# Optimization experiments

Measured on AMD Instinct MI355X. Metric: run time of the kernel, lower is better.

## Reference

```python
import jax, jax.numpy as jnp
import numpy as np
import math

D_MODEL = 1024
N_HEADS = 16
BATCH = 2
SEQ = 2048

def setup_inputs() -> dict:
    key = jax.random.key(0)
    ks = jax.random.split(key, 5)
    d = D_MODEL
    lim_qkv = 1.0 / math.sqrt(d)
    x = jax.random.normal(ks[0], (BATCH, SEQ, d), dtype=jnp.float32)
    qkv_w = jax.random.uniform(ks[1], (3 * d, d), dtype=jnp.float32, minval=-lim_qkv, maxval=lim_qkv)
    qkv_b = jax.random.uniform(ks[2], (3 * d,), dtype=jnp.float32, minval=-lim_qkv, maxval=lim_qkv)
    out_w = jax.random.uniform(ks[3], (d, d), dtype=jnp.float32, minval=-lim_qkv, maxval=lim_qkv)
    out_b = jax.random.uniform(ks[4], (d,), dtype=jnp.float32, minval=-lim_qkv, maxval=lim_qkv)
    return {"x": x, "qkv_w": qkv_w, "qkv_b": qkv_b, "out_w": out_w, "out_b": out_b}

def reference(x, qkv_w, qkv_b, out_w, out_b):
    b, s, d = x.shape
    h = N_HEADS
    hd = d // h
    # note: original uses float division for scale: sqrt(in_features / n_heads)
    scale = math.sqrt(d / h)
    qkv = x @ qkv_w.T + qkv_b                      # [b, s, 3d]
    q, k, v = jnp.split(qkv, 3, axis=-1)           # each [b, s, d]
    def heads(t):
        return t.reshape(b, s, h, hd).transpose(0, 2, 1, 3)  # [b, h, s, hd]
    qh, kh, vh = heads(q), heads(k), heads(v)
    # faithful quirk: scores = k @ q^T (k as query, q as key)
    scores = jnp.einsum('bhid,bhjd->bhij', kh, qh) / scale   # [b, h, s, s]
    alpha = jax.nn.softmax(scores, axis=-1)
    attn = jnp.einsum('bhij,bhjd->bhid', alpha, vh)          # [b, h, s, hd]
    attn = attn.transpose(0, 2, 1, 3).reshape(b, s, d)       # [b, s, d]
    return attn @ out_w.T + out_b
```

## Files before the change

kernel.cpp:

```cpp
#include <hip/hip_runtime.h>
#include <hip/hip_fp16.h>

#define D_MODEL 1024
#define N_HEADS 16
#define HEAD_DIM 64
#define BATCH 2
#define SEQ 2048
#define ROWS (BATCH*SEQ)

#define K_SCALE 0.18033688011112042f

using h8v = __attribute__((ext_vector_type(8))) _Float16;
using h4v = __attribute__((ext_vector_type(4))) _Float16;
using g2v = __attribute__((ext_vector_type(2))) __fp16;
using g4v = __attribute__((ext_vector_type(4))) __fp16;
using us8 = __attribute__((ext_vector_type(8))) unsigned short;
using f4v = __attribute__((ext_vector_type(4))) float;

__device__ __forceinline__ ushort f2h_u(float x) { return __half_as_ushort(__float2half(x)); }
__device__ __forceinline__ void splith(float x, ushort& h, ushort& l) {
    __half hh_ = __float2half(x);
    h = __half_as_ushort(hh_);
    l = f2h_u(x - __half2float(hh_));
}

__device__ __forceinline__ size_t fidx(int row, int k) {
    return ((size_t)((row >> 7) * 32 + (k >> 5)) << 12)
         + (size_t)(((row & 127) >> 4) << 9)
         + (size_t)(((row & 15) * 4 + ((k & 31) >> 3)) << 3) + (k & 7);
}

__device__ __forceinline__ void async_lds16(const ushort* g, ushort* l) {
    __builtin_amdgcn_global_load_lds(
        (const __attribute__((address_space(1))) unsigned int*)g,
        (__attribute__((address_space(3))) unsigned int*)l, 16, 0, 0);
}

__global__ __launch_bounds__(256)
void prep_kernel(const float* __restrict__ x, const float* __restrict__ qw,
                 const float* __restrict__ ow,
                 ushort* __restrict__ xh, ushort* __restrict__ qwh,
                 ushort* __restrict__ owh, ushort* __restrict__ owl)
{
    const int b = blockIdx.x, t = threadIdx.x;
    if (b < 4096) {
        const int i = b * 256 + t;
        const int row = i >> 8, k4 = (i & 255) * 4;
        const float4 v = ((const float4*)x)[i];
        ushort4 h;
        h.x = f2h_u(v.x); h.y = f2h_u(v.y); h.z = f2h_u(v.z); h.w = f2h_u(v.w);
        *(ushort4*)&xh[fidx(row, k4)] = h;
    } else if (b < 7168) {
        const int i = (b - 4096) * 256 + t;
        const int row = i >> 8, k4 = (i & 255) * 4;
        const float4 v = ((const float4*)qw)[i];
        ushort4 h;
        h.x = f2h_u(v.x); h.y = f2h_u(v.y); h.z = f2h_u(v.z); h.w = f2h_u(v.w);
        *(ushort4*)&qwh[fidx(row, k4)] = h;
    } else {
        const int i = (b - 7168) * 256 + t;
        const int row = i >> 8, k4 = (i & 255) * 4;
        const float4 v = ((const float4*)ow)[i];
        const size_t o = fidx(row, k4);
        ushort4 h, l;
        splith(v.x, h.x, l.x); splith(v.y, h.y, l.y);
        splith(v.z, h.z, l.z); splith(v.w, h.w, l.w);
        *(ushort4*)&owh[o] = h; *(ushort4*)&owl[o] = l;
    }
}

__global__ __launch_bounds__(256, 5)
void gemm_qkv(const ushort* __restrict__ Af, const ushort* __restrict__ Wf,
              const float* __restrict__ bias,
              ushort* __restrict__ Qh, ushort* __restrict__ Kh,
              ushort* __restrict__ Vt)
{
    __shared__ ushort sA[2][4096], sW[2][2048];
    const int t = threadIdx.x, lane = t & 63, wv = t >> 6;
    const int tx = lane & 15, g = lane >> 4;
    const int lin = blockIdx.x;
    const int xcd = lin & 7, r = lin >> 3;
    const int mb = xcd * 4 + (r & 3);
    const int nb = r >> 2;
    const int at0 = (wv >> 1) * 4, wt0 = (wv & 1) * 2;
    const int fo = (tx * 4 + g) * 8;
    const size_t wbase = ((size_t)(nb & 1)) << 11;

    f4v acc[8];
#pragma unroll
    for (int i = 0; i < 8; i++)
#pragma unroll
        for (int e = 0; e < 4; e++) acc[i][e] = 0.f;

    {
        const size_t ao = ((size_t)(mb * 32)) << 12;
        const size_t wo = (((size_t)((nb >> 1) * 32)) << 12) + wbase;
#pragma unroll
        for (int c = 0; c < 2; c++) {
            const int o = (t + c * 256) * 8;
            async_lds16(Af + ao + o, &sA[0][o]);
        }
        async_lds16(Wf + wo + t * 8, &sW[0][t * 8]);
    }

    for (int kt = 0; kt < 32; kt++) {
        const int p = kt & 1;
        __syncthreads();
        if (kt < 31) {
            const size_t ao = ((size_t)(mb * 32 + kt + 1)) << 12;
            const size_t wo = (((size_t)((nb >> 1) * 32 + kt + 1)) << 12) + wbase;
#pragma unroll
            for (int c = 0; c < 2; c++) {
                const int o = (t + c * 256) * 8;
                async_lds16(Af + ao + o, &sA[p ^ 1][o]);
            }
            async_lds16(Wf + wo + t * 8, &sW[p ^ 1][t * 8]);
        }
        h8v ah[4], wh[2];
#pragma unroll
        for (int i = 0; i < 4; i++)
            ah[i] = *(const h8v*)&sA[p][(at0 + i) * 512 + fo];
#pragma unroll
        for (int i = 0; i < 2; i++)
            wh[i] = *(const h8v*)&sW[p][(wt0 + i) * 512 + fo];
        if (nb < 32) {
#pragma unroll
            for (int wi = 0; wi < 2; wi++)
#pragma unroll
                for (int ai = 0; ai < 4; ai++)
                    acc[wi * 4 + ai] = __builtin_amdgcn_mfma_f32_16x16x32_f16(wh[wi], ah[ai], acc[wi * 4 + ai], 0, 0, 0);
        } else {
#pragma unroll
            for (int ai = 0; ai < 4; ai++)
#pragma unroll
                for (int wi = 0; wi < 2; wi++)
                    acc[ai * 2 + wi] = __builtin_amdgcn_mfma_f32_16x16x32_f16(ah[ai], wh[wi], acc[ai * 2 + wi], 0, 0, 0);
        }
    }

    if (nb < 32) {
        const int part = nb >> 4;
        ushort* dst = part ? Kh : Qh;
        const float scale = part ? K_SCALE : 1.0f;
#pragma unroll
        for (int wi = 0; wi < 2; wi++) {
            const int gf0 = nb * 64 + (wv & 1) * 32 + wi * 16 + g * 4;
            const float4 bv = *(const float4*)&bias[gf0];
            const int gfl = gf0 & 1023;
            const int hh = gfl >> 6;
            const int dd = gfl & 63;
#pragma unroll
            for (int ai = 0; ai < 4; ai++) {
                const int s = mb * 128 + (wv >> 1) * 64 + ai * 16 + tx;
                const int bb = s >> 11, srel = s & 2047;
                const size_t idx = (size_t)(bb * N_HEADS + hh) * 131072
                    + (size_t)(srel >> 4) * 1024 + (size_t)(dd >> 5) * 512
                    + ((srel & 15) * 4 + ((dd & 31) >> 3)) * 8 + (dd & 7);
                const f4v a = acc[wi * 4 + ai];
                ushort4 h4;
                h4.x = f2h_u((a[0] + bv.x) * scale);
                h4.y = f2h_u((a[1] + bv.y) * scale);
                h4.z = f2h_u((a[2] + bv.z) * scale);
                h4.w = f2h_u((a[3] + bv.w) * scale);
                *(ushort4*)&dst[idx] = h4;
            }
        }
    } else {
#pragma unroll
        for (int wi = 0; wi < 2; wi++) {
            const int gf = nb * 64 + (wv & 1) * 32 + wi * 16 + tx;
            const float bv = bias[gf];
            const int gfl = gf & 1023;
            const int hh = gfl >> 6;
            const int dl = gfl & 63;
            const int t0 = mb * 2 + (wv >> 1);
            const int bb = t0 >> 5;
            const size_t base = (size_t)(bb * N_HEADS + hh) * 131072
                + (size_t)(t0 & 31) * 4096
                + (size_t)((dl >> 4) & 3) * 512
                + (size_t)g * 128 + (size_t)(dl & 15) * 8;
#pragma unroll
            for (int aip = 0; aip < 2; aip++) {
                const f4v a0 = acc[(2 * aip) * 2 + wi];
                const f4v a1 = acc[(2 * aip + 1) * 2 + wi];
                us8 s;
                s[0] = f2h_u(a0[0] + bv); s[1] = f2h_u(a0[1] + bv);
                s[2] = f2h_u(a0[2] + bv); s[3] = f2h_u(a0[3] + bv);
                s[4] = f2h_u(a1[0] + bv); s[5] = f2h_u(a1[1] + bv);
                s[6] = f2h_u(a1[2] + bv); s[7] = f2h_u(a1[3] + bv);
                *(us8*)&Vt[base + (size_t)aip * 2048] = s;
            }
        }
    }
}

__global__ __launch_bounds__(256)
void attn_mfma(const ushort* __restrict__ Kf, const ushort* __restrict__ Qf,
               const ushort* __restrict__ Vf,
               ushort* __restrict__ Oh, ushort* __restrict__ Ol)
{
    __shared__ ushort lds[32768];
    ushort* KR = lds;
    ushort* bufs = lds + 8192;

    const int t = threadIdx.x, lane = t & 63, wv = t >> 6;
    const int tx = lane & 15, g = lane >> 4;
    const int lin = blockIdx.x;
    const int xcd = lin & 7, ix = lin >> 3;
    const int bh = xcd * 4 + (ix >> 4);
    const int it = ix & 15;
    const int b = bh >> 4, h = bh & 15;
    const int i0 = it * 128;
    const size_t hb = (size_t)bh * 131072;

    {
        const size_t kb = hb + (size_t)it * 8192;
#pragma unroll
        for (int c = 0; c < 4; c++) {
            const int o = (t + c * 256) * 8;
            async_lds16(Kf + kb + o, KR + o);
        }
#pragma unroll
        for (int c = 0; c < 2; c++) {
            const int o = (t + c * 256) * 8;
            async_lds16(Qf + hb + o, bufs + o);
            async_lds16(Vf + hb + o, bufs + 4096 + o);
        }
    }
    __syncthreads();

    const int fo = (tx * 4 + g) * 8;
    const int vo = (g * 16 + tx) * 8;
    h8v kf[2][2];
#pragma unroll
    for (int is = 0; is < 2; is++)
#pragma unroll
        for (int kk = 0; kk < 2; kk++)
            kf[is][kk] = *(const h8v*)&KR[((wv * 2 + is) * 2 + kk) * 512 + fo];

    {
        const size_t off = hb + 4096;
#pragma unroll
        for (int c = 0; c < 2; c++) {
            const int o = (t + c * 256) * 8;
            async_lds16(Qf + off + o, bufs + 8192 + o);
            async_lds16(Vf + off + o, bufs + 8192 + 4096 + o);
        }
    }

    f4v O[2][4];
    float l_acc[2] = {0.f, 0.f};
#pragma unroll
    for (int is = 0; is < 2; is++)
#pragma unroll
        for (int ht = 0; ht < 4; ht++)
#pragma unroll
            for (int e = 0; e < 4; e++) O[is][ht][e] = 0.f;

    h4v php[2][4];

    {
        const ushort* sQ = bufs;
        f4v sc[2][4];
#pragma unroll
        for (int is = 0; is < 2; is++)
#pragma unroll
            for (int jn = 0; jn < 4; jn++)
#pragma unroll
                for (int e = 0; e < 4; e++) sc[is][jn][e] = 0.f;
#pragma unroll
        for (int kk = 0; kk < 2; kk++)
#pragma unroll
            for (int jn = 0; jn < 4; jn++) {
                const h8v qf = *(const h8v*)&sQ[(jn * 2 + kk) * 512 + fo];
#pragma unroll
                for (int is = 0; is < 2; is++)
                    sc[is][jn] = __builtin_amdgcn_mfma_f32_16x16x32_f16(qf, kf[is][kk], sc[is][jn], 0, 0, 0);
            }
#pragma unroll
        for (int is = 0; is < 2; is++)
#pragma unroll
            for (int jn = 0; jn < 4; jn++) {
                const float p0 = __builtin_amdgcn_exp2f(sc[is][jn][0]);
                const float p1 = __builtin_amdgcn_exp2f(sc[is][jn][1]);
                const float p2 = __builtin_amdgcn_exp2f(sc[is][jn][2]);
                const float p3 = __builtin_amdgcn_exp2f(sc[is][jn][3]);
                l_acc[is] += (p0 + p1) + (p2 + p3);
                const g2v plo = __builtin_amdgcn_cvt_pkrtz(p0, p1);
                const g2v phi = __builtin_amdgcn_cvt_pkrtz(p2, p3);
                const g4v pk = __builtin_shufflevector(plo, phi, 0, 1, 2, 3);
                php[is][jn] = __builtin_bit_cast(h4v, pk);
            }
    }

    int bp = 0, bc = 1, bn = 2;
    for (int jt = 1; jt < SEQ / 64; jt++) {
        __syncthreads();
        if (jt < SEQ / 64 - 1) {
            const size_t off = hb + (size_t)(jt + 1) * 4096;
#pragma unroll
            for (int c = 0; c < 2; c++) {
                const int o = (t + c * 256) * 8;
                async_lds16(Qf + off + o, bufs + bn * 8192 + o);
                async_lds16(Vf + off + o, bufs + bn * 8192 + 4096 + o);
            }
        }
        const ushort* sQ = bufs + bc * 8192;
        const ushort* sVp = bufs + bp * 8192 + 4096;

        f4v sc[2][4];
#pragma unroll
        for (int is = 0; is < 2; is++)
#pragma unroll
            for (int jn = 0; jn < 4; jn++)
#pragma unroll
                for (int e = 0; e < 4; e++) sc[is][jn][e] = 0.f;
#pragma unroll
        for (int kk = 0; kk < 2; kk++)
#pragma unroll
            for (int jn = 0; jn < 4; jn++) {
                const h8v qf = *(const h8v*)&sQ[(jn * 2 + kk) * 512 + fo];
#pragma unroll
                for (int is = 0; is < 2; is++)
                    sc[is][jn] = __builtin_amdgcn_mfma_f32_16x16x32_f16(qf, kf[is][kk], sc[is][jn], 0, 0, 0);
            }

#pragma unroll
        for (int jc = 0; jc < 2; jc++) {
            h8v p8[2];
#pragma unroll
            for (int is = 0; is < 2; is++)
                p8[is] = __builtin_shufflevector(php[is][jc * 2], php[is][jc * 2 + 1],
                                                 0, 1, 2, 3, 4, 5, 6, 7);
#pragma unroll
            for (int ht = 0; ht < 4; ht++) {
                const h8v vf = *(const h8v*)&sVp[jc * 2048 + ht * 512 + vo];
#pragma unroll
                for (int is = 0; is < 2; is++)
                    O[is][ht] = __builtin_amdgcn_mfma_f32_16x16x32_f16(vf, p8[is], O[is][ht], 0, 0, 0);
            }
        }

#pragma unroll
        for (int is = 0; is < 2; is++)
#pragma unroll
            for (int jn = 0; jn < 4; jn++) {
                const float p0 = __builtin_amdgcn_exp2f(sc[is][jn][0]);
                const float p1 = __builtin_amdgcn_exp2f(sc[is][jn][1]);
                const float p2 = __builtin_amdgcn_exp2f(sc[is][jn][2]);
                const float p3 = __builtin_amdgcn_exp2f(sc[is][jn][3]);
                l_acc[is] += (p0 + p1) + (p2 + p3);
                const g2v plo = __builtin_amdgcn_cvt_pkrtz(p0, p1);
                const g2v phi = __builtin_amdgcn_cvt_pkrtz(p2, p3);
                const g4v pk = __builtin_shufflevector(plo, phi, 0, 1, 2, 3);
                php[is][jn] = __builtin_bit_cast(h4v, pk);
            }

        const int tmp = bp; bp = bc; bc = bn; bn = tmp;
    }

    {
        const ushort* sVp = bufs + bp * 8192 + 4096;
#pragma unroll
        for (int jc = 0; jc < 2; jc++) {
            h8v p8[2];
#pragma unroll
            for (int is = 0; is < 2; is++)
                p8[is] = __builtin_shufflevector(php[is][jc * 2], php[is][jc * 2 + 1],
                                                 0, 1, 2, 3, 4, 5, 6, 7);
#pragma unroll
            for (int ht = 0; ht < 4; ht++) {
                const h8v vf = *(const h8v*)&sVp[jc * 2048 + ht * 512 + vo];
#pragma unroll
                for (int is = 0; is < 2; is++)
                    O[is][ht] = __builtin_amdgcn_mfma_f32_16x16x32_f16(vf, p8[is], O[is][ht], 0, 0, 0);
            }
        }
    }

#pragma unroll
    for (int is = 0; is < 2; is++) {
        float l = l_acc[is];
        l += __shfl_xor(l, 16);
        l += __shfl_xor(l, 32);
        const float inv = 1.0f / l;
        const int row = b * SEQ + i0 + (wv * 2 + is) * 16 + tx;
#pragma unroll
        for (int ht = 0; ht < 4; ht++) {
            const int k0 = h * 64 + ht * 16 + g * 4;
            const size_t o = fidx(row, k0);
            ushort4 hv, lv;
            float v;
            v = O[is][ht][0] * inv; splith(v, hv.x, lv.x);
            v = O[is][ht][1] * inv; splith(v, hv.y, lv.y);
            v = O[is][ht][2] * inv; splith(v, hv.z, lv.z);
            v = O[is][ht][3] * inv; splith(v, hv.w, lv.w);
            *(ushort4*)&Oh[o] = hv;
            *(ushort4*)&Ol[o] = lv;
        }
    }
}

__global__ __launch_bounds__(256, 4)
void gemm_out(const ushort* __restrict__ Af, const ushort* __restrict__ Alf,
              const ushort* __restrict__ Wf, const ushort* __restrict__ Wlf,
              const float* __restrict__ bias, float* __restrict__ out)
{
    __shared__ ushort sA[2][4096], sW[2][4096];
    const int t = threadIdx.x, lane = t & 63, wv = t >> 6;
    const int tx = lane & 15, g = lane >> 4;
    const int lin = blockIdx.x;
    const int xcd = lin & 7, r = lin >> 3;
    const int nb = xcd * 2 + (r & 1);
    const int mb = r >> 1;
    const int at0 = (wv >> 1) * 2, wt0 = (wv & 1) * 2;
    const int fo = (tx * 4 + g) * 8;
    const size_t abase = ((size_t)(mb & 1)) << 11;
    const size_t wbase = ((size_t)(nb & 1)) << 11;

    f4v acc[4];
#pragma unroll
    for (int i = 0; i < 4; i++)
#pragma unroll
        for (int e = 0; e < 4; e++) acc[i][e] = 0.f;

    {
        const size_t ao = (((size_t)((mb >> 1) * 32)) << 12) + abase;
        const size_t wo = (((size_t)((nb >> 1) * 32)) << 12) + wbase;
        const int o = t * 8;
        async_lds16(Af + ao + o, &sA[0][o]);
        async_lds16(Alf + ao + o, &sA[0][2048 + o]);
        async_lds16(Wf + wo + o, &sW[0][o]);
        async_lds16(Wlf + wo + o, &sW[0][2048 + o]);
    }

    for (int kt = 0; kt < 32; kt++) {
        const int p = kt & 1;
        __syncthreads();
        if (kt < 31) {
            const size_t ao = (((size_t)((mb >> 1) * 32 + kt + 1)) << 12) + abase;
            const size_t wo = (((size_t)((nb >> 1) * 32 + kt + 1)) << 12) + wbase;
            const int o = t * 8;
            async_lds16(Af + ao + o, &sA[p ^ 1][o]);
            async_lds16(Alf + ao + o, &sA[p ^ 1][2048 + o]);
            async_lds16(Wf + wo + o, &sW[p ^ 1][o]);
            async_lds16(Wlf + wo + o, &sW[p ^ 1][2048 + o]);
        }
        h8v ah[2], al[2], wh[2], wl[2];
#pragma unroll
        for (int i = 0; i < 2; i++) {
            ah[i] = *(const h8v*)&sA[p][(at0 + i) * 512 + fo];
            al[i] = *(const h8v*)&sA[p][2048 + (at0 + i) * 512 + fo];
            wh[i] = *(const h8v*)&sW[p][(wt0 + i) * 512 + fo];
            wl[i] = *(const h8v*)&sW[p][2048 + (wt0 + i) * 512 + fo];
        }
#pragma unroll
        for (int wi = 0; wi < 2; wi++)
#pragma unroll
            for (int ai = 0; ai < 2; ai++) {
                acc[wi * 2 + ai] = __builtin_amdgcn_mfma_f32_16x16x32_f16(wh[wi], ah[ai], acc[wi * 2 + ai], 0, 0, 0);
                acc[wi * 2 + ai] = __builtin_amdgcn_mfma_f32_16x16x32_f16(wh[wi], al[ai], acc[wi * 2 + ai], 0, 0, 0);
                acc[wi * 2 + ai] = __builtin_amdgcn_mfma_f32_16x16x32_f16(wl[wi], ah[ai], acc[wi * 2 + ai], 0, 0, 0);
            }
    }

#pragma unroll
    for (int wi = 0; wi < 2; wi++) {
        const int gf0 = nb * 64 + (wv & 1) * 32 + wi * 16 + g * 4;
        const float4 bv = *(const float4*)&bias[gf0];
#pragma unroll
        for (int ai = 0; ai < 2; ai++) {
            const int tok = mb * 64 + (wv >> 1) * 32 + ai * 16 + tx;
            const f4v a = acc[wi * 2 + ai];
            float4 o;
            o.x = a[0] + bv.x;
            o.y = a[1] + bv.y;
            o.z = a[2] + bv.z;
            o.w = a[3] + bv.w;
            *(float4*)&out[(size_t)tok * D_MODEL + gf0] = o;
        }
    }
}

extern "C" void kernel_launch(void* const* d_in, const int* in_sizes, int n_in,
                              void* d_out, int out_size, void* d_ws, size_t ws_size,
                              hipStream_t stream) {
    const float* x     = (const float*)d_in[0];
    const float* qkv_w = (const float*)d_in[1];
    const float* qkv_b = (const float*)d_in[2];
    const float* out_w = (const float*)d_in[3];
    const float* out_b = (const float*)d_in[4];
    float* out = (float*)d_out;

    const size_t FB = (size_t)ROWS * D_MODEL;
    const size_t MM = (size_t)D_MODEL * D_MODEL;
    ushort* u   = (ushort*)d_ws;
    ushort* xh  = u;
    ushort* Ol  = u + FB;
    ushort* Qh  = u + 2 * FB;
    ushort* Kh  = u + 3 * FB;
    ushort* Vt  = u + 4 * FB;
    ushort* qwh = u + 5 * FB;
    ushort* owh = u + 5 * FB + 3 * MM;
    ushort* owl = owh + MM;

    prep_kernel<<<8192, 256, 0, stream>>>(x, qkv_w, out_w, xh, qwh, owh, owl);
    gemm_qkv<<<1536, 256, 0, stream>>>(xh, qwh, qkv_b, Qh, Kh, Vt);
    attn_mfma<<<512, 256, 0, stream>>>(Kh, Qh, Vt, xh, Ol);
    gemm_out<<<1024, 256, 0, stream>>>(xh, Ol, owh, owl, out_b, out);
}
```

Before: 208.3 us.

## Fuse fp32-to-fp16 input conversion into QKV GEMM and drop prep kernel

Removes the separate prep kernel that converted x and qkv_w to fp16 in a tiled layout. The QKV GEMM now loads fp32 tiles from global memory into registers, converts them and writes them to LDS, with a register prefetch two tiles ahead. The out_w hi/lo split moves into extra blocks of the same launch. This saves a launch and a full fp16 write and read of x and the weights. In exchange it gives up the async global-to-LDS loads, doubles the global bytes per tile, puts conversion work in the GEMM loop, and lowers occupancy to 4 blocks per CU.

After: 214.0 us. 1.03x slower.

```diff
diff --git a/kernel.cpp b/kernel.cpp
--- a/kernel.cpp
+++ b/kernel.cpp
@@ -36,29 +36,20 @@
         (__attribute__((address_space(3))) unsigned int*)l, 16, 0, 0);
 }
 
-__global__ __launch_bounds__(256)
-void prep_kernel(const float* __restrict__ x, const float* __restrict__ qw,
-                 const float* __restrict__ ow,
-                 ushort* __restrict__ xh, ushort* __restrict__ qwh,
-                 ushort* __restrict__ owh, ushort* __restrict__ owl)
+__global__ __launch_bounds__(256, 4)
+void gemm_qkv(const float* __restrict__ x, const float* __restrict__ qw,
+              const float* __restrict__ bias,
+              ushort* __restrict__ Qh, ushort* __restrict__ Kh,
+              ushort* __restrict__ Vt,
+              const float* __restrict__ ow,
+              ushort* __restrict__ owh, ushort* __restrict__ owl)
 {
-    const int b = blockIdx.x, t = threadIdx.x;
-    if (b < 4096) {
-        const int i = b * 256 + t;
-        const int row = i >> 8, k4 = (i & 255) * 4;
-        const float4 v = ((const float4*)x)[i];
-        ushort4 h;
-        h.x = f2h_u(v.x); h.y = f2h_u(v.y); h.z = f2h_u(v.z); h.w = f2h_u(v.w);
-        *(ushort4*)&xh[fidx(row, k4)] = h;
-    } else if (b < 7168) {
-        const int i = (b - 4096) * 256 + t;
-        const int row = i >> 8, k4 = (i & 255) * 4;
-        const float4 v = ((const float4*)qw)[i];
-        ushort4 h;
-        h.x = f2h_u(v.x); h.y = f2h_u(v.y); h.z = f2h_u(v.z); h.w = f2h_u(v.w);
-        *(ushort4*)&qwh[fidx(row, k4)] = h;
-    } else {
-        const int i = (b - 7168) * 256 + t;
+    __shared__ ushort sA[2][4096], sW[2][2048];
+    const int t = threadIdx.x;
+    const int lin = blockIdx.x;
+
+    if (lin >= 1536) {
+        const int i = (lin - 1536) * 256 + t;
         const int row = i >> 8, k4 = (i & 255) * 4;
         const float4 v = ((const float4*)ow)[i];
         const size_t o = fidx(row, k4);
@@ -66,25 +57,45 @@
         splith(v.x, h.x, l.x); splith(v.y, h.y, l.y);
         splith(v.z, h.z, l.z); splith(v.w, h.w, l.w);
         *(ushort4*)&owh[o] = h; *(ushort4*)&owl[o] = l;
-    }
-}
-
-__global__ __launch_bounds__(256, 5)
-void gemm_qkv(const ushort* __restrict__ Af, const ushort* __restrict__ Wf,
-              const float* __restrict__ bias,
-              ushort* __restrict__ Qh, ushort* __restrict__ Kh,
-              ushort* __restrict__ Vt)
-{
-    __shared__ ushort sA[2][4096], sW[2][2048];
-    const int t = threadIdx.x, lane = t & 63, wv = t >> 6;
+        return;
+    }
+
+    const int lane = t & 63, wv = t >> 6;
     const int tx = lane & 15, g = lane >> 4;
-    const int lin = blockIdx.x;
     const int xcd = lin & 7, r = lin >> 3;
     const int mb = xcd * 4 + (r & 3);
     const int nb = r >> 2;
     const int at0 = (wv >> 1) * 4, wt0 = (wv & 1) * 2;
     const int fo = (tx * 4 + g) * 8;
-    const size_t wbase = ((size_t)(nb & 1)) << 11;
+
+    const int arow = ((t >> 6) * 16) + ((t >> 2) & 15);
+    const int acol = (t & 3) * 8;
+    const float* xbase = x + (size_t)(mb * 128 + arow) * 1024 + acol;
+    const float* wbase = qw + (size_t)(nb * 64 + arow) * 1024 + acol;
+
+    float4 fa0, fa1, fa2, fa3, fw0, fw1;
+    auto ldT = [&](int kt) {
+        const float* xp = xbase + kt * 32;
+        fa0 = *(const float4*)(xp);
+        fa1 = *(const float4*)(xp + 4);
+        fa2 = *(const float4*)(xp + 65536);
+        fa3 = *(const float4*)(xp + 65536 + 4);
+        const float* wp = wbase + kt * 32;
+        fw0 = *(const float4*)(wp);
+        fw1 = *(const float4*)(wp + 4);
+    };
+    auto stT = [&](int p) {
+        us8 a1, a2, w1;
+        a1[0] = f2h_u(fa0.x); a1[1] = f2h_u(fa0.y); a1[2] = f2h_u(fa0.z); a1[3] = f2h_u(fa0.w);
+        a1[4] = f2h_u(fa1.x); a1[5] = f2h_u(fa1.y); a1[6] = f2h_u(fa1.z); a1[7] = f2h_u(fa1.w);
+        a2[0] = f2h_u(fa2.x); a2[1] = f2h_u(fa2.y); a2[2] = f2h_u(fa2.z); a2[3] = f2h_u(fa2.w);
+        a2[4] = f2h_u(fa3.x); a2[5] = f2h_u(fa3.y); a2[6] = f2h_u(fa3.z); a2[7] = f2h_u(fa3.w);
+        w1[0] = f2h_u(fw0.x); w1[1] = f2h_u(fw0.y); w1[2] = f2h_u(fw0.z); w1[3] = f2h_u(fw0.w);
+        w1[4] = f2h_u(fw1.x); w1[5] = f2h_u(fw1.y); w1[6] = f2h_u(fw1.z); w1[7] = f2h_u(fw1.w);
+        *(us8*)&sA[p][t * 8] = a1;
+        *(us8*)&sA[p][2048 + t * 8] = a2;
+        *(us8*)&sW[p][t * 8] = w1;
+    };
 
     f4v acc[8];
 #pragma unroll
@@ -92,29 +103,15 @@
 #pragma unroll
         for (int e = 0; e < 4; e++) acc[i][e] = 0.f;
 
-    {
-        const size_t ao = ((size_t)(mb * 32)) << 12;
-        const size_t wo = (((size_t)((nb >> 1) * 32)) << 12) + wbase;
-#pragma unroll
-        for (int c = 0; c < 2; c++) {
-            const int o = (t + c * 256) * 8;
-            async_lds16(Af + ao + o, &sA[0][o]);
-        }
-        async_lds16(Wf + wo + t * 8, &sW[0][t * 8]);
-    }
+    ldT(0); stT(0);
+    ldT(1);
 
     for (int kt = 0; kt < 32; kt++) {
         const int p = kt & 1;
         __syncthreads();
         if (kt < 31) {
-            const size_t ao = ((size_t)(mb * 32 + kt + 1)) << 12;
-            const size_t wo = (((size_t)((nb >> 1) * 32 + kt + 1)) << 12) + wbase;
-#pragma unroll
-            for (int c = 0; c < 2; c++) {
-                const int o = (t + c * 256) * 8;
-                async_lds16(Af + ao + o, &sA[p ^ 1][o]);
-            }
-            async_lds16(Wf + wo + t * 8, &sW[p ^ 1][t * 8]);
+            stT(p ^ 1);
+            if (kt < 30) ldT(kt + 2);
         }
         h8v ah[4], wh[2];
 #pragma unroll
@@ -495,17 +492,15 @@
     const size_t FB = (size_t)ROWS * D_MODEL;
     const size_t MM = (size_t)D_MODEL * D_MODEL;
     ushort* u   = (ushort*)d_ws;
-    ushort* xh  = u;
+    ushort* Oh  = u;
     ushort* Ol  = u + FB;
     ushort* Qh  = u + 2 * FB;
     ushort* Kh  = u + 3 * FB;
     ushort* Vt  = u + 4 * FB;
-    ushort* qwh = u + 5 * FB;
     ushort* owh = u + 5 * FB + 3 * MM;
     ushort* owl = owh + MM;
 
-    prep_kernel<<<8192, 256, 0, stream>>>(x, qkv_w, out_w, xh, qwh, owh, owl);
-    gemm_qkv<<<1536, 256, 0, stream>>>(xh, qwh, qkv_b, Qh, Kh, Vt);
-    attn_mfma<<<512, 256, 0, stream>>>(Kh, Qh, Vt, xh, Ol);
-    gemm_out<<<1024, 256, 0, stream>>>(xh, Ol, owh, owl, out_b, out);
-}
+    gemm_qkv<<<2560, 256, 0, stream>>>(x, qkv_w, qkv_b, Qh, Kh, Vt, out_w, owh, owl);
+    attn_mfma<<<512, 256, 0, stream>>>(Kh, Qh, Vt, Oh, Ol);
+    gemm_out<<<1024, 256, 0, stream>>>(Oh, Ol, owh, owl, out_b, out);
+}
```

## Move out-proj weight split into QKV GEMM grid and hoist attention LDS loads

Applied to the files above, without the earlier changes.

The out_w hi/lo fp16 split moves from the prep kernel into extra tail blocks of the QKV GEMM launch, so it can overlap with GEMM blocks instead of lengthening the memory-bound prep pass. In the attention inner loop, all V and Q fragments are now loaded from LDS up front, and the PV MFMAs are issued before the score MFMAs so LDS latency is hidden better. This adds register pressure from holding 16 h8v fragments at once. The extra GEMM blocks also share the launch-bounds and LDS footprint of the GEMM kernel.

After: 203.9 us. -2.1%, faster.

```diff
diff --git a/kernel.cpp b/kernel.cpp
--- a/kernel.cpp
+++ b/kernel.cpp
@@ -38,9 +38,7 @@
 
 __global__ __launch_bounds__(256)
 void prep_kernel(const float* __restrict__ x, const float* __restrict__ qw,
-                 const float* __restrict__ ow,
-                 ushort* __restrict__ xh, ushort* __restrict__ qwh,
-                 ushort* __restrict__ owh, ushort* __restrict__ owl)
+                 ushort* __restrict__ xh, ushort* __restrict__ qwh)
 {
     const int b = blockIdx.x, t = threadIdx.x;
     if (b < 4096) {
@@ -50,15 +48,30 @@
         ushort4 h;
         h.x = f2h_u(v.x); h.y = f2h_u(v.y); h.z = f2h_u(v.z); h.w = f2h_u(v.w);
         *(ushort4*)&xh[fidx(row, k4)] = h;
-    } else if (b < 7168) {
+    } else {
         const int i = (b - 4096) * 256 + t;
         const int row = i >> 8, k4 = (i & 255) * 4;
         const float4 v = ((const float4*)qw)[i];
         ushort4 h;
         h.x = f2h_u(v.x); h.y = f2h_u(v.y); h.z = f2h_u(v.z); h.w = f2h_u(v.w);
         *(ushort4*)&qwh[fidx(row, k4)] = h;
-    } else {
-        const int i = (b - 7168) * 256 + t;
+    }
+}
+
+__global__ __launch_bounds__(256, 5)
+void gemm_qkv(const ushort* __restrict__ Af, const ushort* __restrict__ Wf,
+              const float* __restrict__ bias,
+              ushort* __restrict__ Qh, ushort* __restrict__ Kh,
+              ushort* __restrict__ Vt,
+              const float* __restrict__ ow,
+              ushort* __restrict__ owh, ushort* __restrict__ owl)
+{
+    __shared__ ushort sA[2][4096], sW[2][2048];
+    const int t = threadIdx.x;
+    const int lin = blockIdx.x;
+
+    if (lin >= 1536) {
+        const int i = (lin - 1536) * 256 + t;
         const int row = i >> 8, k4 = (i & 255) * 4;
         const float4 v = ((const float4*)ow)[i];
         const size_t o = fidx(row, k4);
@@ -66,19 +79,11 @@
         splith(v.x, h.x, l.x); splith(v.y, h.y, l.y);
         splith(v.z, h.z, l.z); splith(v.w, h.w, l.w);
         *(ushort4*)&owh[o] = h; *(ushort4*)&owl[o] = l;
-    }
-}
-
-__global__ __launch_bounds__(256, 5)
-void gemm_qkv(const ushort* __restrict__ Af, const ushort* __restrict__ Wf,
-              const float* __restrict__ bias,
-              ushort* __restrict__ Qh, ushort* __restrict__ Kh,
-              ushort* __restrict__ Vt)
-{
-    __shared__ ushort sA[2][4096], sW[2][2048];
-    const int t = threadIdx.x, lane = t & 63, wv = t >> 6;
+        return;
+    }
+
+    const int lane = t & 63, wv = t >> 6;
     const int tx = lane & 15, g = lane >> 4;
-    const int lin = blockIdx.x;
     const int xcd = lin & 7, r = lin >> 3;
     const int mb = xcd * 4 + (r & 3);
     const int nb = r >> 2;
@@ -308,22 +313,17 @@
         const ushort* sQ = bufs + bc * 8192;
         const ushort* sVp = bufs + bp * 8192 + 4096;
 
-        f4v sc[2][4];
-#pragma unroll
-        for (int is = 0; is < 2; is++)
+        h8v vf[2][4], qf[2][4];
+#pragma unroll
+        for (int jc = 0; jc < 2; jc++)
+#pragma unroll
+            for (int ht = 0; ht < 4; ht++)
+                vf[jc][ht] = *(const h8v*)&sVp[jc * 2048 + ht * 512 + vo];
+#pragma unroll
+        for (int kk = 0; kk < 2; kk++)
 #pragma unroll
             for (int jn = 0; jn < 4; jn++)
-#pragma unroll
-                for (int e = 0; e < 4; e++) sc[is][jn][e] = 0.f;
-#pragma unroll
-        for (int kk = 0; kk < 2; kk++)
-#pragma unroll
-            for (int jn = 0; jn < 4; jn++) {
-                const h8v qf = *(const h8v*)&sQ[(jn * 2 + kk) * 512 + fo];
-#pragma unroll
-                for (int is = 0; is < 2; is++)
-                    sc[is][jn] = __builtin_amdgcn_mfma_f32_16x16x32_f16(qf, kf[is][kk], sc[is][jn], 0, 0, 0);
-            }
+                qf[kk][jn] = *(const h8v*)&sQ[(jn * 2 + kk) * 512 + fo];
 
 #pragma unroll
         for (int jc = 0; jc < 2; jc++) {
@@ -333,13 +333,26 @@
                 p8[is] = __builtin_shufflevector(php[is][jc * 2], php[is][jc * 2 + 1],
                                                  0, 1, 2, 3, 4, 5, 6, 7);
 #pragma unroll
-            for (int ht = 0; ht < 4; ht++) {
-                const h8v vf = *(const h8v*)&sVp[jc * 2048 + ht * 512 + vo];
+            for (int ht = 0; ht < 4; ht++)
 #pragma unroll
                 for (int is = 0; is < 2; is++)
-                    O[is][ht] = __builtin_amdgcn_mfma_f32_16x16x32_f16(vf, p8[is], O[is][ht], 0, 0, 0);
-            }
-        }
+                    O[is][ht] = __builtin_amdgcn_mfma_f32_16x16x32_f16(vf[jc][ht], p8[is], O[is][ht], 0, 0, 0);
+        }
+
+        f4v sc[2][4];
+#pragma unroll
+        for (int is = 0; is < 2; is++)
+#pragma unroll
+            for (int jn = 0; jn < 4; jn++)
+#pragma unroll
+                for (int e = 0; e < 4; e++) sc[is][jn][e] = 0.f;
+#pragma unroll
+        for (int kk = 0; kk < 2; kk++)
+#pragma unroll
+            for (int jn = 0; jn < 4; jn++)
+#pragma unroll
+                for (int is = 0; is < 2; is++)
+                    sc[is][jn] = __builtin_amdgcn_mfma_f32_16x16x32_f16(qf[kk][jn], kf[is][kk], sc[is][jn], 0, 0, 0);
 
 #pragma unroll
         for (int is = 0; is < 2; is++)
@@ -504,8 +517,8 @@
     ushort* owh = u + 5 * FB + 3 * MM;
     ushort* owl = owh + MM;
 
-    prep_kernel<<<8192, 256, 0, stream>>>(x, qkv_w, out_w, xh, qwh, owh, owl);
-    gemm_qkv<<<1536, 256, 0, stream>>>(xh, qwh, qkv_b, Qh, Kh, Vt);
+    prep_kernel<<<7168, 256, 0, stream>>>(x, qkv_w, xh, qwh);
+    gemm_qkv<<<2560, 256, 0, stream>>>(xh, qwh, qkv_b, Qh, Kh, Vt, out_w, owh, owl);
     attn_mfma<<<512, 256, 0, stream>>>(Kh, Qh, Vt, xh, Ol);
     gemm_out<<<1024, 256, 0, stream>>>(xh, Ol, owh, owl, out_b, out);
 }
```
